# Performance work log

Measured on AMD Instinct MI355X. Metric: run time of the kernel, lower is better.

The kernel has to match this reference:

```python
import jax, jax.numpy as jnp
import numpy as np

DEPTH = 10
NUM_TREES = 64
BATCH = 2048
NUM_FORKS = 2 ** DEPTH - 1  # 1023


def setup_inputs() -> dict:
    key = jax.random.key(0)
    x = jax.random.normal(key, (BATCH, NUM_TREES * NUM_FORKS), dtype=jnp.float32)
    return {"x": x}


def reference(x):
    # [B, T, num_forks]
    logits = x.reshape(-1, NUM_TREES, NUM_FORKS)
    sigmoids = jax.nn.sigmoid(logits)
    # trees_flat: probability mass over current frontier of the tree, starts [B, T, 1]
    trees_flat = jnp.ones_like(logits[:, :, :1])
    j = 0
    trees = None
    for i in range(DEPTH):
        d1 = sigmoids[:, :, j:j + 2 ** i]                 # [B, T, 2^i]
        decisions = jnp.stack([1.0 - d1, d1], axis=3)     # [B, T, 2^i, 2]
        trees = trees_flat[:, :, :, None] * decisions     # [B, T, 2^i, 2]
        trees_flat = trees.reshape(trees.shape[0], NUM_TREES, -1)  # [B, T, 2^(i+1)]
        j += 2 ** i
    # sum over penultimate-level nodes, take right-branch probability
    probabilities = trees.sum(axis=2)                     # [B, T, 2]
    return probabilities[:, :, 1]                         # [B, T]
```

## Files before the change

### kernel.cpp

```cpp
#include <hip/hip_runtime.h>

constexpr int DEPTH      = 10;
constexpr int NUM_TREES  = 64;
constexpr int BATCH      = 2048;
constexpr int NUM_FORKS  = (1 << DEPTH) - 1;
constexpr int PAIRS      = BATCH * NUM_TREES;
constexpr int WPB        = 4;
constexpr int REGION     = 1056;

__device__ __forceinline__ float sig(float v) {
    return __builtin_amdgcn_rcpf(1.0f + __expf(-v));
}

__global__ __launch_bounds__(256, 4) void ndt_kernel(const float* __restrict__ x,
                                                     float* __restrict__ out) {
    __shared__ float lds[WPB * REGION + 8];
    const int tid  = threadIdx.x;
    const int wave = tid >> 6;
    const int lane = tid & 63;
    const int pair = blockIdx.x * WPB + wave;
    const float* __restrict__ xp = x + (size_t)pair * NUM_FORKS;

    float* s = &lds[wave * REGION + 4];

    #pragma unroll
    for (int m = 0; m < 16; ++m) {
        int f = m * 64 + lane;
        if (m < 15 || f < NUM_FORKS) s[1 + f] = xp[f];
    }
    __syncthreads();

    float t9[8];
    #pragma unroll
    for (int c = 0; c < 8; ++c) t9[c] = sig(s[512 + 8 * lane + c]);

    float v8[4];
    #pragma unroll
    for (int d = 0; d < 4; ++d) {
        float sg = sig(s[256 + 4 * lane + d]);
        v8[d] = fmaf(sg, t9[2 * d + 1] - t9[2 * d], t9[2 * d]);
    }

    float v7[2];
    #pragma unroll
    for (int e = 0; e < 2; ++e) {
        float sg = sig(s[128 + 2 * lane + e]);
        v7[e] = fmaf(sg, v8[2 * e + 1] - v8[2 * e], v8[2 * e]);
    }

    float s6 = sig(s[64 + lane]);
    float v6 = fmaf(s6, v7[1] - v7[0], v7[0]);

    float prefix = 1.0f;
    #pragma unroll
    for (int i = 0; i < 6; ++i) {
        int a = lane >> (6 - i);
        int b = (lane >> (5 - i)) & 1;
        float sg = sig(s[(1 << i) + a]);
        prefix *= b ? sg : (1.0f - sg);
    }

    float v = prefix * v6;
    #pragma unroll
    for (int off = 32; off > 0; off >>= 1) v += __shfl_xor(v, off, 64);
    if (lane == 0) out[pair] = v;
}

extern "C" void kernel_launch(void* const* d_in, const int* in_sizes, int n_in,
                              void* d_out, int out_size, void* d_ws, size_t ws_size,
                              hipStream_t stream) {
    const float* x = (const float*)d_in[0];
    float* out = (float*)d_out;
    dim3 grid(PAIRS / WPB), block(WPB * 64);
    ndt_kernel<<<grid, block, 0, stream>>>(x, out);
}
```

Measured before the change: 89.80 us.

## Defer sigmoid reciprocals via rational accumulation and use wave barrier

Rewrites the bottom tree levels to carry numerator/denominator pairs so most sigmoid reciprocals collapse into a few rcp calls, computes the prefix product as one reciprocal of a product of (1+exp) terms, vectorises LDS reads with float4, and replaces __syncthreads with a wave-level barrier since each wave owns its own LDS region. The aim is to cut transcendental instruction count and block-wide sync cost. The risk is overflow or inf in the deferred denominator products when exp terms are large, which can turn results into NaN.

```diff
diff --git a/kernel.cpp b/kernel.cpp
--- a/kernel.cpp
+++ b/kernel.cpp
@@ -8,9 +8,7 @@
 constexpr int WPB        = 4;
 constexpr int REGION     = 1056;
 
-__device__ __forceinline__ float sig(float v) {
-    return __builtin_amdgcn_rcpf(1.0f + __expf(-v));
-}
+constexpr float LOG2E = 1.44269504088896340736f;
 
 __global__ __launch_bounds__(256, 4) void ndt_kernel(const float* __restrict__ x,
                                                      float* __restrict__ out) {
@@ -28,39 +26,54 @@
         int f = m * 64 + lane;
         if (m < 15 || f < NUM_FORKS) s[1 + f] = xp[f];
     }
-    __syncthreads();
+    __builtin_amdgcn_wave_barrier();
 
-    float t9[8];
-    #pragma unroll
-    for (int c = 0; c < 8; ++c) t9[c] = sig(s[512 + 8 * lane + c]);
-
-    float v8[4];
-    #pragma unroll
-    for (int d = 0; d < 4; ++d) {
-        float sg = sig(s[256 + 4 * lane + d]);
-        v8[d] = fmaf(sg, t9[2 * d + 1] - t9[2 * d], t9[2 * d]);
+    float E9[8], D9[8];
+    {
+        const float4 a = *reinterpret_cast<const float4*>(&s[512 + 8 * lane]);
+        const float4 b = *reinterpret_cast<const float4*>(&s[516 + 8 * lane]);
+        const float xs[8] = {a.x, a.y, a.z, a.w, b.x, b.y, b.z, b.w};
+        #pragma unroll
+        for (int c = 0; c < 8; ++c) {
+            E9[c] = __builtin_amdgcn_exp2f(-LOG2E * xs[c]);
+            D9[c] = 1.0f + E9[c];
+        }
     }
-
+    float N8[4], D8[4];
+    {
+        const float4 a = *reinterpret_cast<const float4*>(&s[256 + 4 * lane]);
+        const float xs[4] = {a.x, a.y, a.z, a.w};
+        #pragma unroll
+        for (int d = 0; d < 4; ++d) {
+            float E8 = __builtin_amdgcn_exp2f(-LOG2E * xs[d]);
+            N8[d] = fmaf(E8, D9[2 * d + 1], D9[2 * d]);
+            D8[d] = D9[2 * d] * D9[2 * d + 1] * (1.0f + E8);
+        }
+    }
     float v7[2];
     #pragma unroll
     for (int e = 0; e < 2; ++e) {
-        float sg = sig(s[128 + 2 * lane + e]);
-        v7[e] = fmaf(sg, v8[2 * e + 1] - v8[2 * e], v8[2 * e]);
+        float E7 = __builtin_amdgcn_exp2f(-LOG2E * s[128 + 2 * lane + e]);
+        float N7 = fmaf(E7 * N8[2 * e], D8[2 * e + 1], N8[2 * e + 1] * D8[2 * e]);
+        float D7 = D8[2 * e] * D8[2 * e + 1] * (1.0f + E7);
+        v7[e] = N7 * __builtin_amdgcn_rcpf(D7);
     }
 
-    float s6 = sig(s[64 + lane]);
+    float E6 = __builtin_amdgcn_exp2f(-LOG2E * s[64 + lane]);
+    float s6 = __builtin_amdgcn_rcpf(1.0f + E6);
     float v6 = fmaf(s6, v7[1] - v7[0], v7[0]);
 
-    float prefix = 1.0f;
+    float p = 1.0f;
     #pragma unroll
     for (int i = 0; i < 6; ++i) {
         int a = lane >> (6 - i);
         int b = (lane >> (5 - i)) & 1;
-        float sg = sig(s[(1 << i) + a]);
-        prefix *= b ? sg : (1.0f - sg);
+        float u = LOG2E * s[(1 << i) + a];
+        float w = __builtin_amdgcn_exp2f(b ? -u : u);
+        p *= (1.0f + w);
     }
+    float v = v6 * __builtin_amdgcn_rcpf(p);
 
-    float v = prefix * v6;
     #pragma unroll
     for (int off = 32; off > 0; off >>= 1) v += __shfl_xor(v, off, 64);
     if (lane == 0) out[pair] = v;
```

Measured after the change: 90.20 us. Within noise of the previous version (+0.4%).
